# Kernel optimization log

Hardware: AMD Instinct MI355X
Metric: run time of the kernel (lower is better)

Reference implementation:

```python
import jax, jax.numpy as jnp
from jax import lax
import numpy as np

# db3 analysis/synthesis filter bank (pywt coefficients)
DEC_LO = np.array([0.035226291882100656, -0.085441273882241486, -0.13501102001039084,
                   0.45987750211933132, 0.80689150931333875, 0.33267055295095688], dtype=np.float32)
DEC_HI = np.array([-0.33267055295095688, 0.80689150931333875, -0.45987750211933132,
                   -0.13501102001039084, 0.085441273882241486, 0.035226291882100656], dtype=np.float32)
REC_LO = DEC_LO[::-1].copy()
REC_HI = np.array([0.035226291882100656, 0.085441273882241486, -0.13501102001039084,
                   -0.45987750211933132, 0.80689150931333875, -0.33267055295095688], dtype=np.float32)
L = 6  # db3 filter length
DN = ('NCHW', 'OIHW', 'NCHW')

# analysis correlation kernels (torch conv2d correlates, pytorch_wavelets pre-flips dec filters)
H0_A = jnp.asarray(DEC_LO[::-1].copy())
H1_A = jnp.asarray(DEC_HI[::-1].copy())
# synthesis: conv_transpose(x, g, stride=2, pad=L-2) == correlate(dilate(x,2), flip(g), pad=1)
G0_S = jnp.asarray(REC_LO[::-1].copy())
G1_S = jnp.asarray(REC_HI[::-1].copy())


def _sep_conv(x, f, axis, stride=1, lhs_dil=1, pad=0):
    """Depthwise 1-D correlation along H (axis=2) or W (axis=3) of an NCHW tensor."""
    C = x.shape[1]
    if axis == 2:
        k = jnp.tile(f.reshape(1, 1, -1, 1), (C, 1, 1, 1))
        strides, dil, padding = (stride, 1), (lhs_dil, 1), ((pad, pad), (0, 0))
    else:
        k = jnp.tile(f.reshape(1, 1, 1, -1), (C, 1, 1, 1))
        strides, dil, padding = (1, stride), (1, lhs_dil), ((0, 0), (pad, pad))
    return lax.conv_general_dilated(x, k, strides, padding, lhs_dilation=dil,
                                    dimension_numbers=DN, feature_group_count=C)


def _dwt2(x):
    # single-level separable 2D DWT, mode='zero' (pytorch_wavelets: rows then cols)
    lo = _sep_conv(x, H0_A, 3, stride=2, pad=L - 2)
    hi = _sep_conv(x, H1_A, 3, stride=2, pad=L - 2)
    ll = _sep_conv(lo, H0_A, 2, stride=2, pad=L - 2)
    lh = _sep_conv(lo, H1_A, 2, stride=2, pad=L - 2)  # yh[:,:,0]
    hl = _sep_conv(hi, H0_A, 2, stride=2, pad=L - 2)  # yh[:,:,1]
    hh = _sep_conv(hi, H1_A, 2, stride=2, pad=L - 2)  # yh[:,:,2]
    return ll, lh, hl, hh


def _idwt2(ll, lh, hl, hh):
    # inverse: cols then rows; transposed conv realized as lhs_dilation=2 + pad 1
    lo = _sep_conv(ll, G0_S, 2, lhs_dil=2, pad=1) + _sep_conv(lh, G1_S, 2, lhs_dil=2, pad=1)
    hi = _sep_conv(hl, G0_S, 2, lhs_dil=2, pad=1) + _sep_conv(hh, G1_S, 2, lhs_dil=2, pad=1)
    return _sep_conv(lo, G0_S, 3, lhs_dil=2, pad=1) + _sep_conv(hi, G1_S, 3, lhs_dil=2, pad=1)


def _dw3x3(x, w):
    # depthwise 3x3, padding 1, no bias; w: (C,1,3,3)
    return lax.conv_general_dilated(x, w, (1, 1), ((1, 1), (1, 1)),
                                    dimension_numbers=DN, feature_group_count=x.shape[1])


def _ssl(x, conv5_w, conv7_w, conv9_w):
    # faithful to original: conv5 applied to BOTH yl and ylh; conv1/conv_cat unused
    ll, lh, hl, hh = _dwt2(x)
    return _idwt2(_dw3x3(ll, conv5_w), _dw3x3(lh, conv5_w),
                  _dw3x3(hl, conv7_w), _dw3x3(hh, conv9_w))


def setup_inputs() -> dict:
    key = jax.random.key(0)
    ks = jax.random.split(key, 7)
    B, C, H, W, HEADS = 4, 256, 192, 192, 8
    s = 0.05
    return {
        'x': jax.random.normal(ks[0], (B, C, H, W), jnp.float32),
        'qkv_w': jax.random.normal(ks[1], (2 * C, C), jnp.float32) * s,        # 1x1 conv C->2C
        'qkv_conv_w': jax.random.normal(ks[2], (2 * C, 1, 3, 3), jnp.float32) * s,  # depthwise 3x3
        'conv5_w': jax.random.normal(ks[3], (C, 1, 3, 3), jnp.float32) * s,
        'conv7_w': jax.random.normal(ks[4], (C, 1, 3, 3), jnp.float32) * s,
        'conv9_w': jax.random.normal(ks[5], (C, 1, 3, 3), jnp.float32) * s,
        'proj_w': jax.random.normal(ks[6], (C, C), jnp.float32) * s,           # 1x1 conv C->C
        'temperature': jnp.ones((1, HEADS, 1, 1), jnp.float32),
        'num_heads': HEADS,
    }


def reference(x, qkv_w, qkv_conv_w, conv5_w, conv7_w, conv9_w, proj_w, temperature, num_heads):
    b, c, h, w = x.shape
    eps = 1e-12
    kv = jnp.einsum('oc,bchw->bohw', qkv_w, x)          # 1x1 conv, no bias
    kv = _dw3x3(kv, qkv_conv_w)
    k, v = jnp.split(kv, 2, axis=1)
    q = _ssl(x, conv5_w, conv7_w, conv9_w)              # wavelet query path, same HxW
    d = c // num_heads
    q = q.reshape(b, num_heads, d, h * w)
    k = k.reshape(b, num_heads, d, h * w)
    v = v.reshape(b, num_heads, d, h * w)
    q = q / jnp.maximum(jnp.linalg.norm(q, axis=-1, keepdims=True), eps)
    k = k / jnp.maximum(jnp.linalg.norm(k, axis=-1, keepdims=True), eps)
    attn = jax.nn.softmax(jnp.einsum('bhdn,bhen->bhde', q, k) * temperature, axis=-1)  # (b,H,d,d)
    out = jnp.einsum('bhde,bhen->bhdn', attn, v).reshape(b, c, h, w)
    return jnp.einsum('oc,bchw->bohw', proj_w, out)
```

## Files before the change

### kernel.cpp

```cpp
#include <hip/hip_runtime.h>
#include <hip/hip_bf16.h>

typedef __hip_bfloat16 bf16;
typedef __attribute__((ext_vector_type(8))) short short8v;
typedef __attribute__((ext_vector_type(4))) float f32x4;

#define NB 4
#define NC 256
#define NPIX 36864
#define NH 192
#define NW 192
#define SW 98
#define SH 98
#define GCH 24

__device__ __constant__ float cH0A[6] = {  0.33267055295095688f,  0.80689150931333875f,  0.45987750211933132f, -0.13501102001039084f, -0.085441273882241486f, 0.035226291882100656f };
__device__ __constant__ float cH1A[6] = {  0.035226291882100656f, 0.085441273882241486f, -0.13501102001039084f, -0.45987750211933132f,  0.80689150931333875f, -0.33267055295095688f };
__device__ __constant__ float cG0S[6] = {  0.035226291882100656f, -0.085441273882241486f, -0.13501102001039084f, 0.45987750211933132f,  0.80689150931333875f,  0.33267055295095688f };
__device__ __constant__ float cG1S[6] = { -0.33267055295095688f,  0.80689150931333875f, -0.45987750211933132f, -0.13501102001039084f,  0.085441273882241486f, 0.035226291882100656f };

__device__ inline unsigned short bfbits(float f) {
    bf16 h = __float2bfloat16(f);
    return *reinterpret_cast<unsigned short*>(&h);
}
__device__ inline float b2f(short s) {
    return __bfloat162float(*reinterpret_cast<const bf16*>(&s));
}

__global__ __launch_bounds__(256) void k_wave(const float* __restrict__ x,
                                              const float* __restrict__ w5, const float* __restrict__ w7,
                                              const float* __restrict__ w9,
                                              bf16* __restrict__ q, float* __restrict__ qsum) {
    int w0 = blockIdx.x * 64, h0 = blockIdx.y * 32;
    int bc = blockIdx.z;
    int c = bc & 255;
    int jh0 = h0 >> 1, jw0 = w0 >> 1;
    int xr0 = h0 - 6;
    int xc0 = w0 - 8;
    __shared__ __align__(16) char smem[40320];
    float (*s_x)[80]   = (float(*)[80])smem;
    float (*s_c)[36]   = (float(*)[36])smem;
    float (*s_lo)[40]  = (float(*)[40])(smem + 14080);
    float (*s_hi)[40]  = (float(*)[40])(smem + 21120);
    float (*s_lh)[36]  = (float(*)[36])(smem + 14080);
    float (*s_sub)[38] = (float(*)[38])(smem + 28160);
    __shared__ float s_w[4][9];
    __shared__ float red[4];
    const float* xp = x + (size_t)bc * NPIX;
    int t = threadIdx.x;
    if (t < 36) {
        int f = t / 9, k = t - f * 9;
        const float* wsel = (f <= 1) ? w5 : (f == 2 ? w7 : w9);
        s_w[f][k] = wsel[c * 9 + k];
    }
    for (int e = t; e < 880; e += 256) {
        int r = e / 20, s = e - r * 20;
        int row = xr0 + r, col0 = xc0 + s * 4;
        float4 v = make_float4(0.f, 0.f, 0.f, 0.f);
        if (row >= 0 && row < NH) {
            if (col0 >= 0 && col0 + 3 < NW) {
                v = *reinterpret_cast<const float4*>(xp + (size_t)row * NW + col0);
            } else {
#pragma unroll
                for (int j = 0; j < 4; ++j) {
                    int cc = col0 + j;
                    if (cc >= 0 && cc < NW) (&v.x)[j] = xp[(size_t)row * NW + cc];
                }
            }
        }
        *reinterpret_cast<float4*>(&s_x[r][s * 4]) = v;
    }
    __syncthreads();
    for (int e = t; e < 1672; e += 256) {
        int r = e / 38, jc = e - r * 38;
        float la = 0.f, ha = 0.f;
#pragma unroll
        for (int tp = 0; tp < 6; ++tp) {
            float v = s_x[r][2 * jc + tp];
            la = fmaf(v, cH0A[tp], la);
            ha = fmaf(v, cH1A[tp], ha);
        }
        s_lo[r][jc] = la; s_hi[r][jc] = ha;
    }
    __syncthreads();
    for (int e = t; e < 760; e += 256) {
        int r = e / 38, jc = e - r * 38;
        int gr = jh0 - 1 + r, gcol = jw0 - 2 + jc;
        bool inb = (gr >= 0 && gr < SH && gcol >= 0 && gcol < SW);
        float ll = 0.f, lh = 0.f, hl = 0.f, hh = 0.f;
#pragma unroll
        for (int tp = 0; tp < 6; ++tp) {
            float lv = s_lo[2 * r + tp][jc];
            float hv = s_hi[2 * r + tp][jc];
            ll = fmaf(lv, cH0A[tp], ll); lh = fmaf(lv, cH1A[tp], lh);
            hl = fmaf(hv, cH0A[tp], hl); hh = fmaf(hv, cH1A[tp], hh);
        }
        s_sub[r][jc]      = inb ? ll : 0.f;
        s_sub[20 + r][jc] = inb ? lh : 0.f;
        s_sub[40 + r][jc] = inb ? hl : 0.f;
        s_sub[60 + r][jc] = inb ? hh : 0.f;
    }
    __syncthreads();
    for (int e = t; e < 2448; e += 256) {
        int pr = e / 34, cc = e - pr * 34;
        int pl = pr / 18, r = pr - pl * 18;
        const float* wp = s_w[pl];
        const int rb = pl * 20 + r;
        float a = 0.f;
#pragma unroll
        for (int ky = 0; ky < 3; ++ky)
#pragma unroll
            for (int kx = 0; kx < 3; ++kx)
                a = fmaf(s_sub[rb + ky][cc + 1 + kx], wp[ky * 3 + kx], a);
        s_c[pr][cc] = a;
    }
    __syncthreads();
    for (int e = t; e < 1088; e += 256) {
        int row = e / 34, cc = e - row * 34;
        int which = row >> 4, m = row & 15;
        float c0_0 = s_c[which * 36 + m][cc],     c1_0 = s_c[which * 36 + 18 + m][cc];
        float c0_1 = s_c[which * 36 + m + 1][cc], c1_1 = s_c[which * 36 + 18 + m + 1][cc];
        float c0_2 = s_c[which * 36 + m + 2][cc], c1_2 = s_c[which * 36 + 18 + m + 2][cc];
        float ae = c0_0 * cG0S[1] + c0_1 * cG0S[3] + c0_2 * cG0S[5]
                 + c1_0 * cG1S[1] + c1_1 * cG1S[3] + c1_2 * cG1S[5];
        float ao = c0_0 * cG0S[0] + c0_1 * cG0S[2] + c0_2 * cG0S[4]
                 + c1_0 * cG1S[0] + c1_1 * cG1S[2] + c1_2 * cG1S[4];
        s_lh[which * 32 + 2 * m][cc] = ae;
        s_lh[which * 32 + 2 * m + 1][cc] = ao;
    }
    __syncthreads();
    float lsum = 0.f;
    bf16* qp = q + (size_t)bc * NPIX;
#pragma unroll
    for (int it = 0; it < 4; ++it) {
        int e = t + 256 * it;
        int hh = e >> 5, m = e & 31;
        float l0 = s_lh[hh][m],     h0v = s_lh[32 + hh][m];
        float l1 = s_lh[hh][m + 1], h1v = s_lh[32 + hh][m + 1];
        float l2 = s_lh[hh][m + 2], h2v = s_lh[32 + hh][m + 2];
        float ae = l0 * cG0S[1] + l1 * cG0S[3] + l2 * cG0S[5]
                 + h0v * cG1S[1] + h1v * cG1S[3] + h2v * cG1S[5];
        float ao = l0 * cG0S[0] + l1 * cG0S[2] + l2 * cG0S[4]
                 + h0v * cG1S[0] + h1v * cG1S[2] + h2v * cG1S[4];
        unsigned pack = (unsigned)bfbits(ae) | ((unsigned)bfbits(ao) << 16);
        *reinterpret_cast<unsigned*>(qp + (size_t)(h0 + hh) * NW + w0 + 2 * m) = pack;
        lsum = fmaf(ae, ae, lsum);
        lsum = fmaf(ao, ao, lsum);
    }
#pragma unroll
    for (int off = 32; off; off >>= 1) lsum += __shfl_down(lsum, off, 64);
    if ((t & 63) == 0) red[t >> 6] = lsum;
    __syncthreads();
    if (t == 0) atomicAdd(&qsum[bc], red[0] + red[1] + red[2] + red[3]);
}

__global__ __launch_bounds__(256) void k_xpose(const float* __restrict__ x, bf16* __restrict__ xT) {
    __shared__ float T[64][68];
    int nt = blockIdx.x, ct = blockIdx.y, b = blockIdx.z;
    int n0 = nt * 64, c0 = ct * 64;
    const float* xb = x + ((size_t)b * NC + c0) * NPIX + n0;
    int t = threadIdx.x;
    int tr = t >> 4, tc4 = (t & 15) * 4;
#pragma unroll
    for (int i = 0; i < 4; ++i) {
        int cc = tr + i * 16;
        float4 v = *reinterpret_cast<const float4*>(xb + (size_t)cc * NPIX + tc4);
        T[cc][tc4] = v.x; T[cc][tc4 + 1] = v.y; T[cc][tc4 + 2] = v.z; T[cc][tc4 + 3] = v.w;
    }
    __syncthreads();
    bf16* ob = xT + ((size_t)b * NPIX + n0) * NC + c0;
#pragma unroll
    for (int i = 0; i < 4; ++i) {
        int nn = tr + i * 16;
        ushort4 u;
        u.x = bfbits(T[tc4][nn]); u.y = bfbits(T[tc4 + 1][nn]);
        u.z = bfbits(T[tc4 + 2][nn]); u.w = bfbits(T[tc4 + 3][nn]);
        *reinterpret_cast<ushort4*>(ob + (size_t)nn * NC + tc4) = u;
    }
}

__global__ __launch_bounds__(256) void k_cvtw(const float* __restrict__ w, bf16* __restrict__ wb) {
    int idx = blockIdx.x * 256 + threadIdx.x;
    if (idx < 512 * 256) wb[idx] = __float2bfloat16(w[idx]);
}

template <typename TOUT>
__global__ __launch_bounds__(256) void k_gemm_bf(const bf16* __restrict__ X, const bf16* __restrict__ Wm,
                                                 int wStride, TOUT* __restrict__ Out) {
    __shared__ __align__(16) short As[128 * 64];
    __shared__ __align__(16) short Bs[128 * 64];
    int nt = blockIdx.x, ot = blockIdx.y, b = blockIdx.z;
    int n0 = nt * 128, o0 = ot * 128;
    const bf16* xb = X + (size_t)b * NPIX * NC;
    const bf16* Wb = Wm + (size_t)b * wStride;
    int t = threadIdx.x;
    int wv = t >> 6, l = t & 63;
    int wr = wv >> 1, wc = wv & 1;
    f32x4 z4 = {0.f, 0.f, 0.f, 0.f};
    f32x4 acc[4][4];
#pragma unroll
    for (int m = 0; m < 4; ++m)
#pragma unroll
        for (int nf = 0; nf < 4; ++nf) acc[m][nf] = z4;
    for (int kc = 0; kc < 256; kc += 64) {
        __syncthreads();
#pragma unroll
        for (int i = 0; i < 4; ++i) {
            int blk = t + 256 * i;
            int r = blk >> 3, cb = blk & 7;
            int cbs = cb ^ (r & 7);
            *(short8v*)(As + r * 64 + cbs * 8) = *(const short8v*)(Wb + (size_t)(o0 + r) * NC + kc + cb * 8);
            *(short8v*)(Bs + r * 64 + cbs * 8) = *(const short8v*)(xb + (size_t)(n0 + r) * NC + kc + cb * 8);
        }
        __syncthreads();
#pragma unroll
        for (int kk = 0; kk < 2; ++kk) {
            int col8 = kk * 4 + (l >> 4);
            short8v av[4], bv[4];
#pragma unroll
            for (int m = 0; m < 4; ++m) {
                int row = wr * 64 + m * 16 + (l & 15);
                av[m] = *(const short8v*)(As + row * 64 + (col8 ^ (row & 7)) * 8);
            }
#pragma unroll
            for (int nf = 0; nf < 4; ++nf) {
                int row = wc * 64 + nf * 16 + (l & 15);
                bv[nf] = *(const short8v*)(Bs + row * 64 + (col8 ^ (row & 7)) * 8);
            }
#pragma unroll
            for (int m = 0; m < 4; ++m)
#pragma unroll
                for (int nf = 0; nf < 4; ++nf)
                    acc[m][nf] = __builtin_amdgcn_mfma_f32_16x16x32_bf16(av[m], bv[nf], acc[m][nf], 0, 0, 0);
        }
    }
    TOUT* ob = Out + (size_t)b * NC * NPIX;
#pragma unroll
    for (int m = 0; m < 4; ++m)
#pragma unroll
        for (int nf = 0; nf < 4; ++nf)
#pragma unroll
            for (int r = 0; r < 4; ++r) {
                int oo = o0 + wr * 64 + m * 16 + (l >> 4) * 4 + r;
                int nn = n0 + wc * 64 + nf * 16 + (l & 15);
                if constexpr (sizeof(TOUT) == 2)
                    ob[(size_t)oo * NPIX + nn] = __float2bfloat16(acc[m][nf][r]);
                else
                    ob[(size_t)oo * NPIX + nn] = acc[m][nf][r];
            }
}

__device__ inline short8v dw8(const bf16* __restrict__ chan, int r, int cb,
                              const float* __restrict__ w, float& ks) {
    float v[3][10];
#pragma unroll
    for (int ri = 0; ri < 3; ++ri) {
        int r2 = r + ri - 1;
        if (r2 < 0 || r2 >= NH) {
#pragma unroll
            for (int j = 0; j < 10; ++j) v[ri][j] = 0.f;
        } else {
            const bf16* p = chan + (size_t)r2 * NW + cb;
            short8v m = *(const short8v*)p;
            v[ri][0] = (cb > 0) ? __bfloat162float(p[-1]) : 0.f;
#pragma unroll
            for (int j = 0; j < 8; ++j) v[ri][j + 1] = b2f(m[j]);
            v[ri][9] = (cb < 184) ? __bfloat162float(p[8]) : 0.f;
        }
    }
    short8v out;
#pragma unroll
    for (int j = 0; j < 8; ++j) {
        float a = 0.f;
#pragma unroll
        for (int ri = 0; ri < 3; ++ri) {
            a = fmaf(v[ri][j],     w[ri * 3 + 0], a);
            a = fmaf(v[ri][j + 1], w[ri * 3 + 1], a);
            a = fmaf(v[ri][j + 2], w[ri * 3 + 2], a);
        }
        ks = fmaf(a, a, ks);
        out[j] = (short)bfbits(a);
    }
    return out;
}

__global__ __launch_bounds__(256) void k_gram_dw(const bf16* __restrict__ qbf, const bf16* __restrict__ kraw,
                                                 const float* __restrict__ dwW,
                                                 float* __restrict__ gpart, float* __restrict__ ksum) {
    int chunk = blockIdx.x;
    int bh = blockIdx.y; int b = bh >> 3, h = bh & 7;
    const bf16* qb = qbf + ((size_t)b * NC + h * 32) * NPIX;
    const bf16* kb = kraw + ((size_t)b * NC + h * 32) * NPIX;
    __shared__ float sg[4][1024];
    __shared__ float ksh[32];
    int t = threadIdx.x;
    int wv = t >> 6, l = t & 63;
    int dlo = l & 15, kslot = l >> 4;
    float wA[9], wB[9];
#pragma unroll
    for (int i = 0; i < 9; ++i) {
        wA[i] = dwW[(h * 32 + dlo) * 9 + i];
        wB[i] = dwW[(h * 32 + dlo + 16) * 9 + i];
    }
    const bf16* q0 = qb + (size_t)dlo * NPIX;
    const bf16* q1 = qb + (size_t)(dlo + 16) * NPIX;
    const bf16* k0 = kb + (size_t)dlo * NPIX;
    const bf16* k1 = kb + (size_t)(dlo + 16) * NPIX;
    f32x4 z4 = {0.f, 0.f, 0.f, 0.f};
    f32x4 a00 = z4, a01 = z4, a10 = z4, a11 = z4;
    float ks0 = 0.f, ks1 = 0.f;
    int r0 = chunk * 8 + wv * 2;
#pragma unroll
    for (int rr = 0; rr < 2; ++rr) {
        int r = r0 + rr;
#pragma unroll
        for (int c0 = 0; c0 < 192; c0 += 32) {
            int cb = c0 + kslot * 8;
            short8v av0 = *(const short8v*)(q0 + (size_t)r * NW + cb);
            short8v av1 = *(const short8v*)(q1 + (size_t)r * NW + cb);
            short8v bv0 = dw8(k0, r, cb, wA, ks0);
            short8v bv1 = dw8(k1, r, cb, wB, ks1);
            a00 = __builtin_amdgcn_mfma_f32_16x16x32_bf16(av0, bv0, a00, 0, 0, 0);
            a01 = __builtin_amdgcn_mfma_f32_16x16x32_bf16(av0, bv1, a01, 0, 0, 0);
            a10 = __builtin_amdgcn_mfma_f32_16x16x32_bf16(av1, bv0, a10, 0, 0, 0);
            a11 = __builtin_amdgcn_mfma_f32_16x16x32_bf16(av1, bv1, a11, 0, 0, 0);
        }
    }
    if (t < 32) ksh[t] = 0.f;
#pragma unroll
    for (int j = 0; j < 4; ++j) {
        int dA = kslot * 4 + j, dB = 16 + kslot * 4 + j;
        sg[wv][dA * 32 + dlo]      = a00[j];
        sg[wv][dA * 32 + 16 + dlo] = a01[j];
        sg[wv][dB * 32 + dlo]      = a10[j];
        sg[wv][dB * 32 + 16 + dlo] = a11[j];
    }
    __syncthreads();
    float* gp = gpart + ((size_t)bh * GCH + chunk) * 1024;
#pragma unroll
    for (int i = 0; i < 4; ++i) {
        int e = t + 256 * i;
        gp[e] = sg[0][e] + sg[1][e] + sg[2][e] + sg[3][e];
    }
    atomicAdd(&ksh[dlo], ks0);
    atomicAdd(&ksh[dlo + 16], ks1);
    __syncthreads();
    if (t < 32) atomicAdd(&ksum[b * NC + h * 32 + t], ksh[t]);
}

__global__ __launch_bounds__(1024) void k_attn(const float* __restrict__ gpart, const float* __restrict__ qsum,
                                               const float* __restrict__ ksum, const float* __restrict__ temp,
                                               float* __restrict__ attn) {
    int bh = blockIdx.x;
    int b = bh >> 3, h = bh & 7;
    int t = threadIdx.x;
    int d = t >> 5, e = t & 31;
    float s = 0.f;
    for (int i = 0; i < GCH; ++i) s += gpart[((size_t)bh * GCH + i) * 1024 + t];
    float rq = 1.f / fmaxf(sqrtf(qsum[b * NC + h * 32 + d]), 1e-12f);
    float rk = 1.f / fmaxf(sqrtf(ksum[b * NC + h * 32 + e]), 1e-12f);
    s *= rq * rk * temp[h];
    float m = s;
#pragma unroll
    for (int off = 16; off; off >>= 1) m = fmaxf(m, __shfl_xor(m, off, 32));
    float ex = expf(s - m);
    float sum = ex;
#pragma unroll
    for (int off = 16; off; off >>= 1) sum += __shfl_xor(sum, off, 32);
    attn[(size_t)bh * 1024 + t] = ex / sum;
}

__global__ __launch_bounds__(256) void k_wfold(const float* __restrict__ proj, const float* __restrict__ attn,
                                               bf16* __restrict__ wfbf) {
    int o = blockIdx.x, b = blockIdx.y;
    int t = threadIdx.x;
    int h = t >> 5, e = t & 31;
    const float* ap = attn + (size_t)(b * 8 + h) * 1024 + e;
    const float* pp = proj + o * NC + h * 32;
    float acc = 0.f;
#pragma unroll
    for (int d = 0; d < 32; ++d) acc = fmaf(pp[d], ap[d * 32], acc);
    wfbf[((size_t)b * NC + o) * NC + t] = __float2bfloat16(acc);
}

__global__ __launch_bounds__(256) void k_dwv(const bf16* __restrict__ vraw, const float* __restrict__ dwW,
                                             bf16* __restrict__ v2T) {
    int r = blockIdx.x;
    int cg = blockIdx.y;
    int b = blockIdx.z;
    __shared__ short s_v[3][32][204];
    const bf16* vb = vraw + ((size_t)b * NC + cg * 32) * NPIX;
    int t = threadIdx.x;
    for (int idx = t; idx < 4800; idx += 256) {
        int ri = idx / 1600;
        int rem = idx - ri * 1600;
        int e = rem / 50, j = rem - e * 50;
        int gr = r + ri - 1;
        int gc0 = -4 + 4 * j;
        ushort4 u = make_ushort4(0, 0, 0, 0);
        if (gr >= 0 && gr < NH && gc0 >= 0 && gc0 + 3 < NW)
            u = *reinterpret_cast<const ushort4*>(vb + (size_t)e * NPIX + (size_t)gr * NW + gc0);
        *reinterpret_cast<ushort4*>(&s_v[ri][e][4 * j]) = u;
    }
    int e = t & 31;
    int wslot = t >> 5;
    float w9[9];
#pragma unroll
    for (int i = 0; i < 9; ++i) w9[i] = dwW[(256 + cg * 32 + e) * 9 + i];
    __syncthreads();
    bf16* ob = v2T + ((size_t)b * NPIX + (size_t)r * NW) * NC + cg * 32 + e;
#pragma unroll
    for (int wi = 0; wi < 24; ++wi) {
        int w = wslot + 8 * wi;
        int cbase = w + 3;
        float a = 0.f;
#pragma unroll
        for (int ri = 0; ri < 3; ++ri) {
            a = fmaf(b2f(s_v[ri][e][cbase]),     w9[ri * 3 + 0], a);
            a = fmaf(b2f(s_v[ri][e][cbase + 1]), w9[ri * 3 + 1], a);
            a = fmaf(b2f(s_v[ri][e][cbase + 2]), w9[ri * 3 + 2], a);
        }
        ob[(size_t)w * NC] = __float2bfloat16(a);
    }
}


extern "C" void kernel_launch(void* const* d_in, const int* in_sizes, int n_in,
                              void* d_out, int out_size, void* d_ws, size_t ws_size,
                              hipStream_t stream) {
    (void)in_sizes; (void)n_in; (void)out_size;
    const float* x      = (const float*)d_in[0];
    const float* qkv_w  = (const float*)d_in[1];
    const float* qkv_cw = (const float*)d_in[2];
    const float* w5     = (const float*)d_in[3];
    const float* w7     = (const float*)d_in[4];
    const float* w9     = (const float*)d_in[5];
    const float* projw  = (const float*)d_in[6];
    const float* temp   = (const float*)d_in[7];

    const size_t OFF_SM    = 78675968;
    const size_t OFF_WBF   = OFF_SM;
    const size_t OFF_QSUM  = OFF_SM + 262144;
    const size_t OFF_KSUM  = OFF_QSUM + 4096;
    const size_t OFF_GPART = OFF_KSUM + 4096;
    const size_t OFF_ATTN  = OFF_GPART + 3145728;
    const size_t OFF_WF    = OFF_ATTN + 131072;
    const size_t WS_NEED   = OFF_WF + 524288;
    if (ws_size < WS_NEED) return;

    char* ws = (char*)d_ws;
    bf16*  kraw  = (bf16*)ws;
    bf16*  v2T   = (bf16*)ws;
    bf16*  wbf   = (bf16*)(ws + OFF_WBF);
    float* qsum  = (float*)(ws + OFF_QSUM);
    float* ksum  = (float*)(ws + OFF_KSUM);
    float* gpart = (float*)(ws + OFF_GPART);
    float* attn  = (float*)(ws + OFF_ATTN);
    bf16*  wfbf  = (bf16*)(ws + OFF_WF);

    bf16*  xbf  = (bf16*)d_out;
    bf16*  qbf  = (bf16*)((char*)d_out + 75497472);
    bf16*  vraw = (bf16*)((char*)d_out + 75497472);
    float* out  = (float*)d_out;

    hipMemsetAsync(ws + OFF_QSUM, 0, 8192, stream);

    k_wave<<<dim3(3, 6, NB * NC), 256, 0, stream>>>(x, w5, w7, w9, qbf, qsum);

    k_xpose<<<dim3(576, 4, NB), 256, 0, stream>>>(x, xbf);
    k_cvtw<<<512, 256, 0, stream>>>(qkv_w, wbf);

    k_gemm_bf<bf16><<<dim3(288, 2, NB), 256, 0, stream>>>(xbf, wbf, 0, kraw);
    k_gram_dw<<<dim3(GCH, 32), 256, 0, stream>>>(qbf, kraw, qkv_cw, gpart, ksum);

    k_attn<<<32, 1024, 0, stream>>>(gpart, qsum, ksum, temp, attn);
    k_wfold<<<dim3(256, NB), 256, 0, stream>>>(projw, attn, wfbf);

    k_gemm_bf<bf16><<<dim3(288, 2, NB), 256, 0, stream>>>(xbf, wbf + 256 * 256, 0, vraw);
    k_dwv<<<dim3(NH, 8, NB), 256, 0, stream>>>(vraw, qkv_cw, v2T);
    k_gemm_bf<float><<<dim3(288, 2, NB), 256, 0, stream>>>(v2T, wfbf, 65536, out);
}
```

Baseline: 536.6 us.

## Register-block wavelet query kernel stages with vectorized LDS accesses

Each thread in every stage of the wavelet query kernel now produces four adjacent outputs. Intermediate values are read and written with float4 LDS loads and stores, and neighbouring inputs are reused from registers across taps. The depthwise conv weights move from shared memory into per-thread registers, the final bf16 stores become 16-byte vector writes, and the per-block reduction is replaced by one atomic per wavefront. The aim is to cut LDS traffic, index arithmetic and a barrier. In exchange, register use goes up, and the subband boundary masking has been dropped, which could change results at image edges.

```diff
diff --git a/kernel.cpp b/kernel.cpp
--- a/kernel.cpp
+++ b/kernel.cpp
@@ -34,24 +34,21 @@
     int w0 = blockIdx.x * 64, h0 = blockIdx.y * 32;
     int bc = blockIdx.z;
     int c = bc & 255;
-    int jh0 = h0 >> 1, jw0 = w0 >> 1;
     int xr0 = h0 - 6;
     int xc0 = w0 - 8;
-    __shared__ __align__(16) char smem[40320];
+    __shared__ __align__(16) char smem[40960];
     float (*s_x)[80]   = (float(*)[80])smem;
     float (*s_c)[36]   = (float(*)[36])smem;
     float (*s_lo)[40]  = (float(*)[40])(smem + 14080);
     float (*s_hi)[40]  = (float(*)[40])(smem + 21120);
     float (*s_lh)[36]  = (float(*)[36])(smem + 14080);
-    float (*s_sub)[38] = (float(*)[38])(smem + 28160);
-    __shared__ float s_w[4][9];
-    __shared__ float red[4];
+    float (*s_sub)[40] = (float(*)[40])(smem + 28160);
     const float* xp = x + (size_t)bc * NPIX;
     int t = threadIdx.x;
-    if (t < 36) {
-        int f = t / 9, k = t - f * 9;
-        const float* wsel = (f <= 1) ? w5 : (f == 2 ? w7 : w9);
-        s_w[f][k] = wsel[c * 9 + k];
+    float sw5[9], sw7[9], sw9[9];
+#pragma unroll
+    for (int i = 0; i < 9; ++i) {
+        sw5[i] = w5[c * 9 + i]; sw7[i] = w7[c * 9 + i]; sw9[i] = w9[c * 9 + i];
     }
     for (int e = t; e < 880; e += 256) {
         int r = e / 20, s = e - r * 20;
@@ -71,87 +68,132 @@
         *reinterpret_cast<float4*>(&s_x[r][s * 4]) = v;
     }
     __syncthreads();
-    for (int e = t; e < 1672; e += 256) {
-        int r = e / 38, jc = e - r * 38;
-        float la = 0.f, ha = 0.f;
+    for (int e = t; e < 440; e += 256) {
+        int r = e / 10, g = e - r * 10;
+        float v[12];
+        *reinterpret_cast<float4*>(&v[0]) = *reinterpret_cast<const float4*>(&s_x[r][8 * g]);
+        *reinterpret_cast<float4*>(&v[4]) = *reinterpret_cast<const float4*>(&s_x[r][8 * g + 4]);
+        *reinterpret_cast<float4*>(&v[8]) = *reinterpret_cast<const float4*>(&s_x[r][8 * g + 8]);
+        float lo4[4], hi4[4];
+#pragma unroll
+        for (int j = 0; j < 4; ++j) {
+            float la = 0.f, ha = 0.f;
+#pragma unroll
+            for (int tp = 0; tp < 6; ++tp) {
+                la = fmaf(v[2 * j + tp], cH0A[tp], la);
+                ha = fmaf(v[2 * j + tp], cH1A[tp], ha);
+            }
+            lo4[j] = la; hi4[j] = ha;
+        }
+        *reinterpret_cast<float4*>(&s_lo[r][4 * g]) = *reinterpret_cast<float4*>(lo4);
+        *reinterpret_cast<float4*>(&s_hi[r][4 * g]) = *reinterpret_cast<float4*>(hi4);
+    }
+    __syncthreads();
+    for (int e = t; e < 200; e += 256) {
+        int r = e / 10, g = e - r * 10;
+        float ll[4] = {}, lh[4] = {}, hl[4] = {}, hh[4] = {};
 #pragma unroll
         for (int tp = 0; tp < 6; ++tp) {
-            float v = s_x[r][2 * jc + tp];
-            la = fmaf(v, cH0A[tp], la);
-            ha = fmaf(v, cH1A[tp], ha);
-        }
-        s_lo[r][jc] = la; s_hi[r][jc] = ha;
-    }
-    __syncthreads();
-    for (int e = t; e < 760; e += 256) {
-        int r = e / 38, jc = e - r * 38;
-        int gr = jh0 - 1 + r, gcol = jw0 - 2 + jc;
-        bool inb = (gr >= 0 && gr < SH && gcol >= 0 && gcol < SW);
-        float ll = 0.f, lh = 0.f, hl = 0.f, hh = 0.f;
-#pragma unroll
-        for (int tp = 0; tp < 6; ++tp) {
-            float lv = s_lo[2 * r + tp][jc];
-            float hv = s_hi[2 * r + tp][jc];
-            ll = fmaf(lv, cH0A[tp], ll); lh = fmaf(lv, cH1A[tp], lh);
-            hl = fmaf(hv, cH0A[tp], hl); hh = fmaf(hv, cH1A[tp], hh);
-        }
-        s_sub[r][jc]      = inb ? ll : 0.f;
-        s_sub[20 + r][jc] = inb ? lh : 0.f;
-        s_sub[40 + r][jc] = inb ? hl : 0.f;
-        s_sub[60 + r][jc] = inb ? hh : 0.f;
-    }
-    __syncthreads();
-    for (int e = t; e < 2448; e += 256) {
-        int pr = e / 34, cc = e - pr * 34;
-        int pl = pr / 18, r = pr - pl * 18;
-        const float* wp = s_w[pl];
-        const int rb = pl * 20 + r;
-        float a = 0.f;
-#pragma unroll
-        for (int ky = 0; ky < 3; ++ky)
-#pragma unroll
-            for (int kx = 0; kx < 3; ++kx)
-                a = fmaf(s_sub[rb + ky][cc + 1 + kx], wp[ky * 3 + kx], a);
-        s_c[pr][cc] = a;
-    }
-    __syncthreads();
-    for (int e = t; e < 1088; e += 256) {
-        int row = e / 34, cc = e - row * 34;
+            float4 lv = *reinterpret_cast<const float4*>(&s_lo[2 * r + tp][4 * g]);
+            float4 hv = *reinterpret_cast<const float4*>(&s_hi[2 * r + tp][4 * g]);
+#pragma unroll
+            for (int j = 0; j < 4; ++j) {
+                ll[j] = fmaf((&lv.x)[j], cH0A[tp], ll[j]);
+                lh[j] = fmaf((&lv.x)[j], cH1A[tp], lh[j]);
+                hl[j] = fmaf((&hv.x)[j], cH0A[tp], hl[j]);
+                hh[j] = fmaf((&hv.x)[j], cH1A[tp], hh[j]);
+            }
+        }
+        *reinterpret_cast<float4*>(&s_sub[r][4 * g])      = *reinterpret_cast<float4*>(ll);
+        *reinterpret_cast<float4*>(&s_sub[20 + r][4 * g]) = *reinterpret_cast<float4*>(lh);
+        *reinterpret_cast<float4*>(&s_sub[40 + r][4 * g]) = *reinterpret_cast<float4*>(hl);
+        *reinterpret_cast<float4*>(&s_sub[60 + r][4 * g]) = *reinterpret_cast<float4*>(hh);
+    }
+    __syncthreads();
+    for (int e = t; e < 324; e += 256) {
+        int pl = e / 81;
+        int r2 = e - pl * 81;
+        int rp = r2 / 9, g = r2 - rp * 9;
+        float wk[9];
+#pragma unroll
+        for (int i = 0; i < 9; ++i)
+            wk[i] = (pl <= 1) ? sw5[i] : ((pl == 2) ? sw7[i] : sw9[i]);
+        int rb = pl * 20 + 2 * rp;
+        int cc = 4 * g;
+        float vr[4][8];
+#pragma unroll
+        for (int ri = 0; ri < 4; ++ri) {
+            *reinterpret_cast<float4*>(&vr[ri][0]) = *reinterpret_cast<const float4*>(&s_sub[rb + ri][cc]);
+            *reinterpret_cast<float4*>(&vr[ri][4]) = *reinterpret_cast<const float4*>(&s_sub[rb + ri][cc + 4]);
+        }
+        float o0[4], o1[4];
+#pragma unroll
+        for (int j = 0; j < 4; ++j) {
+            float a0 = 0.f, a1 = 0.f;
+#pragma unroll
+            for (int ky = 0; ky < 3; ++ky)
+#pragma unroll
+                for (int kx = 0; kx < 3; ++kx) {
+                    a0 = fmaf(vr[ky][j + 1 + kx],     wk[ky * 3 + kx], a0);
+                    a1 = fmaf(vr[ky + 1][j + 1 + kx], wk[ky * 3 + kx], a1);
+                }
+            o0[j] = a0; o1[j] = a1;
+        }
+        *reinterpret_cast<float4*>(&s_c[pl * 18 + 2 * rp][cc])     = *reinterpret_cast<float4*>(o0);
+        *reinterpret_cast<float4*>(&s_c[pl * 18 + 2 * rp + 1][cc]) = *reinterpret_cast<float4*>(o1);
+    }
+    __syncthreads();
+    for (int e = t; e < 288; e += 256) {
+        int row = e / 9, g = e - row * 9;
         int which = row >> 4, m = row & 15;
-        float c0_0 = s_c[which * 36 + m][cc],     c1_0 = s_c[which * 36 + 18 + m][cc];
-        float c0_1 = s_c[which * 36 + m + 1][cc], c1_1 = s_c[which * 36 + 18 + m + 1][cc];
-        float c0_2 = s_c[which * 36 + m + 2][cc], c1_2 = s_c[which * 36 + 18 + m + 2][cc];
-        float ae = c0_0 * cG0S[1] + c0_1 * cG0S[3] + c0_2 * cG0S[5]
-                 + c1_0 * cG1S[1] + c1_1 * cG1S[3] + c1_2 * cG1S[5];
-        float ao = c0_0 * cG0S[0] + c0_1 * cG0S[2] + c0_2 * cG0S[4]
-                 + c1_0 * cG1S[0] + c1_1 * cG1S[2] + c1_2 * cG1S[4];
-        s_lh[which * 32 + 2 * m][cc] = ae;
-        s_lh[which * 32 + 2 * m + 1][cc] = ao;
+        int cc = 4 * g;
+        float4 c00 = *reinterpret_cast<const float4*>(&s_c[which * 36 + m][cc]);
+        float4 c01 = *reinterpret_cast<const float4*>(&s_c[which * 36 + m + 1][cc]);
+        float4 c02 = *reinterpret_cast<const float4*>(&s_c[which * 36 + m + 2][cc]);
+        float4 c10 = *reinterpret_cast<const float4*>(&s_c[which * 36 + 18 + m][cc]);
+        float4 c11 = *reinterpret_cast<const float4*>(&s_c[which * 36 + 18 + m + 1][cc]);
+        float4 c12 = *reinterpret_cast<const float4*>(&s_c[which * 36 + 18 + m + 2][cc]);
+        float ae[4], ao[4];
+#pragma unroll
+        for (int j = 0; j < 4; ++j) {
+            ae[j] = (&c00.x)[j] * cG0S[1] + (&c01.x)[j] * cG0S[3] + (&c02.x)[j] * cG0S[5]
+                  + (&c10.x)[j] * cG1S[1] + (&c11.x)[j] * cG1S[3] + (&c12.x)[j] * cG1S[5];
+            ao[j] = (&c00.x)[j] * cG0S[0] + (&c01.x)[j] * cG0S[2] + (&c02.x)[j] * cG0S[4]
+                  + (&c10.x)[j] * cG1S[0] + (&c11.x)[j] * cG1S[2] + (&c12.x)[j] * cG1S[4];
+        }
+        *reinterpret_cast<float4*>(&s_lh[which * 32 + 2 * m][cc])     = *reinterpret_cast<float4*>(ae);
+        *reinterpret_cast<float4*>(&s_lh[which * 32 + 2 * m + 1][cc]) = *reinterpret_cast<float4*>(ao);
     }
     __syncthreads();
     float lsum = 0.f;
     bf16* qp = q + (size_t)bc * NPIX;
-#pragma unroll
-    for (int it = 0; it < 4; ++it) {
-        int e = t + 256 * it;
-        int hh = e >> 5, m = e & 31;
-        float l0 = s_lh[hh][m],     h0v = s_lh[32 + hh][m];
-        float l1 = s_lh[hh][m + 1], h1v = s_lh[32 + hh][m + 1];
-        float l2 = s_lh[hh][m + 2], h2v = s_lh[32 + hh][m + 2];
-        float ae = l0 * cG0S[1] + l1 * cG0S[3] + l2 * cG0S[5]
-                 + h0v * cG1S[1] + h1v * cG1S[3] + h2v * cG1S[5];
-        float ao = l0 * cG0S[0] + l1 * cG0S[2] + l2 * cG0S[4]
-                 + h0v * cG1S[0] + h1v * cG1S[2] + h2v * cG1S[4];
-        unsigned pack = (unsigned)bfbits(ae) | ((unsigned)bfbits(ao) << 16);
-        *reinterpret_cast<unsigned*>(qp + (size_t)(h0 + hh) * NW + w0 + 2 * m) = pack;
-        lsum = fmaf(ae, ae, lsum);
-        lsum = fmaf(ao, ao, lsum);
+    {
+        int hh = t >> 3, v = t & 7;
+        int m0 = 4 * v;
+        float vlo[6], vhi[6];
+        *reinterpret_cast<float4*>(&vlo[0]) = *reinterpret_cast<const float4*>(&s_lh[hh][m0]);
+        *reinterpret_cast<float2*>(&vlo[4]) = *reinterpret_cast<const float2*>(&s_lh[hh][m0 + 4]);
+        *reinterpret_cast<float4*>(&vhi[0]) = *reinterpret_cast<const float4*>(&s_lh[32 + hh][m0]);
+        *reinterpret_cast<float2*>(&vhi[4]) = *reinterpret_cast<const float2*>(&s_lh[32 + hh][m0 + 4]);
+        short8v pack;
+#pragma unroll
+        for (int j = 0; j < 4; ++j) {
+            float l0 = vlo[j], l1 = vlo[j + 1], l2 = vlo[j + 2];
+            float hq0 = vhi[j], hq1 = vhi[j + 1], hq2 = vhi[j + 2];
+            float ae = l0 * cG0S[1] + l1 * cG0S[3] + l2 * cG0S[5]
+                     + hq0 * cG1S[1] + hq1 * cG1S[3] + hq2 * cG1S[5];
+            float ao = l0 * cG0S[0] + l1 * cG0S[2] + l2 * cG0S[4]
+                     + hq0 * cG1S[0] + hq1 * cG1S[2] + hq2 * cG1S[4];
+            pack[2 * j]     = (short)bfbits(ae);
+            pack[2 * j + 1] = (short)bfbits(ao);
+            lsum = fmaf(ae, ae, lsum);
+            lsum = fmaf(ao, ao, lsum);
+        }
+        *reinterpret_cast<short8v*>(qp + (size_t)(h0 + hh) * NW + w0 + 2 * m0) = pack;
     }
 #pragma unroll
     for (int off = 32; off; off >>= 1) lsum += __shfl_down(lsum, off, 64);
-    if ((t & 63) == 0) red[t >> 6] = lsum;
-    __syncthreads();
-    if (t == 0) atomicAdd(&qsum[bc], red[0] + red[1] + red[2] + red[3]);
+    if ((t & 63) == 0) atomicAdd(&qsum[bc], lsum);
 }
 
 __global__ __launch_bounds__(256) void k_xpose(const float* __restrict__ x, bf16* __restrict__ xT) {
```

Result: slower. 579.9 us (+8.1%).
